# Kernel tuning notes

Measured on AMD Instinct MI355X. Metric: run time of the kernel, lower is better.

The kernel has to match this reference:

```python
import jax, jax.numpy as jnp
import numpy as np

S = 8192          # past KV length
H = 4096          # hidden size
NH = 32           # heads
HD = 128          # head dim
INNER = 16384     # MLP inner (4h)
ROT = 64          # rotary dim per 2D-rope half
NUM_LAYERS = 28
LAYER_ID = 0
ALPHA = (2.0 * NUM_LAYERS) ** 0.5
QK_COEFF = float(LAYER_ID + 1)            # query_key_layer_scaling_coeff
COEFF = (128.0 ** 0.5) * QK_COEFF         # math.sqrt(128) * coeff
EPS = 1e-5


def layernorm(x, w, b):
    mu = jnp.mean(x, axis=-1, keepdims=True)
    var = jnp.var(x, axis=-1, keepdims=True)
    return (x - mu) * jax.lax.rsqrt(var + EPS) * w + b


def rotate_half(x):
    # x: [..., 64]; GLM rotate-half at 32
    return jnp.concatenate([-x[..., 32:], x[..., :32]], axis=-1)


def setup_inputs() -> dict:
    key = jax.random.key(0)
    ks = jax.random.split(key, 16)
    # rotary cache (as in the driver script)
    inv_freq = 1.0 / (10000.0 ** (jnp.arange(0, ROT, 2, dtype=jnp.float32) / ROT))  # [32]
    t = jnp.arange(512, dtype=jnp.float32)
    freqs = jnp.einsum('i,j->ij', t, inv_freq)          # [512,32]
    emb = jnp.concatenate([freqs, freqs], axis=-1)      # [512,64]
    w = lambda k, shp: jax.random.normal(k, shp, dtype=jnp.float32) * 0.02
    return {
        'hidden_states': jax.random.normal(ks[0], (1, H), dtype=jnp.float32),
        'past_key': jax.random.normal(ks[1], (S, NH, HD), dtype=jnp.float32),
        'past_value': jax.random.normal(ks[2], (S, NH, HD), dtype=jnp.float32),
        'cos_cached': jnp.cos(emb),
        'sin_cached': jnp.sin(emb),
        'ln1_w': jnp.ones((H,), jnp.float32), 'ln1_b': jnp.zeros((H,), jnp.float32),
        'qkv_w': w(ks[3], (3 * H, H)), 'qkv_b': w(ks[4], (3 * H,)),
        'dense_w': w(ks[5], (H, H)), 'dense_b': w(ks[6], (H,)),
        'ln2_w': jnp.ones((H,), jnp.float32), 'ln2_b': jnp.zeros((H,), jnp.float32),
        'fc1_w': w(ks[7], (INNER, H)), 'fc1_b': w(ks[8], (INNER,)),
        'fc2_w': w(ks[9], (H, INNER)), 'fc2_b': w(ks[10], (H,)),
        'position_ids': jax.random.randint(ks[11], (1, 1), 0, 512),
        'block_position_ids': jax.random.randint(ks[12], (1, 1), 0, 512),
        'attention_mask': jnp.zeros((1, 1, S + 1), dtype=bool),
    }


def reference(hidden_states, past_key, past_value, cos_cached, sin_cached,
              ln1_w, ln1_b, qkv_w, qkv_b, dense_w, dense_b,
              ln2_w, ln2_b, fc1_w, fc1_b, fc2_w, fc2_b,
              position_ids, block_position_ids, attention_mask):
    # rotary lookups: embedding then transpose(0,1) -> [q_len,1,64]
    pos_cos = jnp.transpose(cos_cached[position_ids], (1, 0, 2))
    pos_sin = jnp.transpose(sin_cached[position_ids], (1, 0, 2))
    blk_cos = jnp.transpose(cos_cached[block_position_ids], (1, 0, 2))
    blk_sin = jnp.transpose(sin_cached[block_position_ids], (1, 0, 2))

    residual = layernorm(hidden_states, ln1_w, ln1_b)          # [1, H]
    qkv = residual @ qkv_w.T + qkv_b                           # [1, 3H]
    qkv = qkv.reshape(-1, NH, 3 * HD)                          # [1, 32, 384]
    query, key_new, value_new = jnp.split(qkv, 3, axis=2)      # each [1,32,128]

    q1, q2 = jnp.split(query, 2, axis=2)                       # [1,32,64] each
    k1, k2 = jnp.split(key_new, 2, axis=2)
    q1 = q1 * pos_cos + rotate_half(q1) * pos_sin
    k1 = k1 * pos_cos + rotate_half(k1) * pos_sin
    q2 = q2 * blk_cos + rotate_half(q2) * blk_sin
    k2 = k2 * blk_cos + rotate_half(k2) * blk_sin
    q = jnp.concatenate([q1, q2], axis=-1)                     # [1,32,128]
    k_new = jnp.concatenate([k1, k2], axis=-1)                 # [1,32,128]

    k = jnp.concatenate([past_key, k_new], axis=0)             # [S+1,32,128]
    v = jnp.concatenate([past_value, value_new], axis=0)       # [S+1,32,128]

    # scores: [heads, q=1, S+1]
    scores = jnp.einsum('qhd,khd->hqk', q / COEFF, k)
    scores = jnp.where(attention_mask, jnp.float32(-10000.0), scores)
    scores = scores * QK_COEFF
    probs = jax.nn.softmax(scores, axis=-1)
    ctx = jnp.einsum('hqk,khd->qhd', probs, v).reshape(-1, H)  # [1,4096]

    attn_out = ctx @ dense_w.T + dense_b
    hidden = residual * ALPHA + attn_out

    residual2 = layernorm(hidden, ln2_w, ln2_b)
    mlp = jax.nn.gelu(residual2 @ fc1_w.T + fc1_b, approximate=True)
    mlp = mlp @ fc2_w.T + fc2_b
    out = residual2 * ALPHA + mlp
    return (out, k, v)
```

## Files before the change

kernel.cpp:

```cpp
#include <hip/hip_runtime.h>
#include <math.h>

#define S_PAST 8192
#define S_TOT  8193
#define HID    4096
#define NH     32
#define HD     128
#define INNER  16384
#define CH     16
#define NCH    512
#define ALPHA_ 7.483314773547883f
#define INV_COEFF 0.08838834764831845f
#define EPS_ 1e-5f

__global__ __launch_bounds__(256) void ln_kernel(const float* __restrict__ xin,
                                                 const float* __restrict__ w,
                                                 const float* __restrict__ b,
                                                 float* __restrict__ out) {
    int tid = threadIdx.x;
    float xs[16];
    float s = 0.f, s2 = 0.f;
#pragma unroll
    for (int i = 0; i < 16; ++i) {
        float v = xin[tid + i * 256];
        xs[i] = v; s += v; s2 += v * v;
    }
    for (int off = 32; off; off >>= 1) {
        s  += __shfl_down(s, off, 64);
        s2 += __shfl_down(s2, off, 64);
    }
    __shared__ float rs[4], rs2[4];
    __shared__ float mu_s, ri_s;
    int wid = tid >> 6, lane = tid & 63;
    if (lane == 0) { rs[wid] = s; rs2[wid] = s2; }
    __syncthreads();
    if (tid == 0) {
        float S1 = rs[0] + rs[1] + rs[2] + rs[3];
        float S2 = rs2[0] + rs2[1] + rs2[2] + rs2[3];
        float mu = S1 / HID;
        float var = S2 / HID - mu * mu;
        mu_s = mu;
        ri_s = rsqrtf(var + EPS_);
    }
    __syncthreads();
    float mu = mu_s, ri = ri_s;
#pragma unroll
    for (int i = 0; i < 16; ++i) {
        int idx = tid + i * 256;
        out[idx] = (xs[i] - mu) * ri * w[idx] + b[idx];
    }
}

template <int C, int MODE>
__global__ __launch_bounds__(256) void gemv_kernel(
        const float* __restrict__ Wm, const float* __restrict__ bias,
        const float* __restrict__ x, float* __restrict__ y,
        const float* __restrict__ res) {
    int wid = threadIdx.x >> 6, lane = threadIdx.x & 63;
    int r = blockIdx.x * 4 + wid;
    const float4* __restrict__ rowv = (const float4*)(Wm + (size_t)r * C);
    const float4* __restrict__ xv = (const float4*)x;
    constexpr int IT = C / 4 / 64;
    float acc0 = 0.f, acc1 = 0.f;
#pragma unroll 8
    for (int it = 0; it < IT; it += 2) {
        float4 w0 = rowv[lane + it * 64];
        float4 x0 = xv[lane + it * 64];
        float4 w1 = rowv[lane + (it + 1) * 64];
        float4 x1 = xv[lane + (it + 1) * 64];
        acc0 += w0.x * x0.x + w0.y * x0.y + w0.z * x0.z + w0.w * x0.w;
        acc1 += w1.x * x1.x + w1.y * x1.y + w1.z * x1.z + w1.w * x1.w;
    }
    float acc = acc0 + acc1;
    for (int off = 32; off; off >>= 1) acc += __shfl_down(acc, off, 64);
    if (lane == 0) {
        float t = acc + bias[r];
        if (MODE == 1) t += ALPHA_ * res[r];
        if (MODE == 2) {
            float u = t;
            t = 0.5f * u * (1.f + tanhf(0.7978845608028654f * (u + 0.044715f * u * u * u)));
        }
        y[r] = t;
    }
}

__global__ __launch_bounds__(256) void gemv_wide_kernel(
        const float* __restrict__ Wm, const float* __restrict__ bias,
        const float* __restrict__ x, float* __restrict__ y,
        const float* __restrict__ res) {
    int tid = threadIdx.x;
    int r = blockIdx.x;
    const float4* __restrict__ rowv = (const float4*)(Wm + (size_t)r * INNER);
    const float4* __restrict__ xv = (const float4*)x;
    float acc0 = 0.f, acc1 = 0.f;
#pragma unroll 8
    for (int it = 0; it < 16; it += 2) {
        float4 w0 = rowv[tid + it * 256];
        float4 x0 = xv[tid + it * 256];
        float4 w1 = rowv[tid + (it + 1) * 256];
        float4 x1 = xv[tid + (it + 1) * 256];
        acc0 += w0.x * x0.x + w0.y * x0.y + w0.z * x0.z + w0.w * x0.w;
        acc1 += w1.x * x1.x + w1.y * x1.y + w1.z * x1.z + w1.w * x1.w;
    }
    float acc = acc0 + acc1;
    for (int off = 32; off; off >>= 1) acc += __shfl_down(acc, off, 64);
    __shared__ float red[4];
    int wid = tid >> 6, lane = tid & 63;
    if (lane == 0) red[wid] = acc;
    __syncthreads();
    if (tid == 0) {
        float t = red[0] + red[1] + red[2] + red[3] + bias[r];
        t += ALPHA_ * res[r];
        y[r] = t;
    }
}

__global__ __launch_bounds__(128) void rope_kv_kernel(
        const float* __restrict__ qkv, const float* __restrict__ cosc,
        const float* __restrict__ sinc, const int* __restrict__ pos_ids,
        const int* __restrict__ blk_ids, float* __restrict__ qrot,
        float* __restrict__ kout, float* __restrict__ vout) {
    int h = blockIdx.x, d = threadIdx.x;
    int pos = pos_ids[0], blk = blk_ids[0];
    const float* qh = qkv + h * 384;
    float q = qh[d], k = qh[128 + d], v = qh[256 + d];
    int half = d >> 6;
    int i = d & 63;
    int p = half ? blk : pos;
    float c = cosc[p * 64 + i];
    float s = sinc[p * 64 + i];
    float qpart, kpart;
    int base = half * 64;
    if (i < 32) { qpart = -qh[base + i + 32]; kpart = -qh[128 + base + i + 32]; }
    else        { qpart =  qh[base + i - 32]; kpart =  qh[128 + base + i - 32]; }
    float qo = q * c + qpart * s;
    float ko = k * c + kpart * s;
    qrot[h * HD + d] = qo * INV_COEFF;
    size_t o = (size_t)S_PAST * HID + h * HD + d;
    kout[o] = ko;
    vout[o] = v;
}

__global__ __launch_bounds__(512) void attn_onepass(
        const float* __restrict__ qrot, const float* __restrict__ pastk,
        const float* __restrict__ pastv, float* __restrict__ kout,
        float* __restrict__ vout, const unsigned char* __restrict__ mask,
        float* __restrict__ pctx, float* __restrict__ pL) {
    int tid = threadIdx.x;
    int t = tid & 255, u = tid >> 8;
    int s0 = blockIdx.x * CH;
    int rows = (blockIdx.x == NCH - 1) ? (S_TOT - s0) : CH;
    int rstart = u * 8;
    int rend = u ? rows : 8;
    int a = t >> 5;
    const float4* __restrict__ qv = (const float4*)qrot;
    float4 q0 = qv[t], q1 = qv[256 + t], q2 = qv[512 + t], q3 = qv[768 + t];
    float4 a0 = {0,0,0,0}, a1 = {0,0,0,0}, a2 = {0,0,0,0}, a3 = {0,0,0,0};
    float eL0 = 0.f, eL1 = 0.f, eL2 = 0.f, eL3 = 0.f;
#pragma unroll 4
    for (int r = rstart; r < rend; ++r) {
        int srow = s0 + r;
        bool past = srow < S_PAST;
        const float* kbase = past ? pastk : kout;
        const float* vbase = past ? pastv : vout;
        const float4* krow = (const float4*)(kbase + (size_t)srow * HID);
        const float4* vrow = (const float4*)(vbase + (size_t)srow * HID);
        float4 k0 = krow[t], k1 = krow[256 + t];
        float4 k2 = krow[512 + t], k3 = krow[768 + t];
        float4 v0 = vrow[t], v1 = vrow[256 + t];
        float4 v2 = vrow[512 + t], v3 = vrow[768 + t];
        if (past) {
            float4* ko = (float4*)(kout + (size_t)srow * HID);
            ko[t] = k0; ko[256 + t] = k1; ko[512 + t] = k2; ko[768 + t] = k3;
            float4* vo = (float4*)(vout + (size_t)srow * HID);
            vo[t] = v0; vo[256 + t] = v1; vo[512 + t] = v2; vo[768 + t] = v3;
        }
        float d0 = q0.x * k0.x + q0.y * k0.y + q0.z * k0.z + q0.w * k0.w;
        float d1 = q1.x * k1.x + q1.y * k1.y + q1.z * k1.z + q1.w * k1.w;
        float d2 = q2.x * k2.x + q2.y * k2.y + q2.z * k2.z + q2.w * k2.w;
        float d3 = q3.x * k3.x + q3.y * k3.y + q3.z * k3.z + q3.w * k3.w;
#pragma unroll
        for (int off = 1; off < 32; off <<= 1) {
            d0 += __shfl_xor(d0, off, 64);
            d1 += __shfl_xor(d1, off, 64);
            d2 += __shfl_xor(d2, off, 64);
            d3 += __shfl_xor(d3, off, 64);
        }
        if (mask[srow]) { d0 = d1 = d2 = d3 = -10000.f; }
        float p0 = __expf(d0), p1 = __expf(d1), p2 = __expf(d2), p3 = __expf(d3);
        eL0 += p0; eL1 += p1; eL2 += p2; eL3 += p3;
        a0.x += p0 * v0.x; a0.y += p0 * v0.y; a0.z += p0 * v0.z; a0.w += p0 * v0.w;
        a1.x += p1 * v1.x; a1.y += p1 * v1.y; a1.z += p1 * v1.z; a1.w += p1 * v1.w;
        a2.x += p2 * v2.x; a2.y += p2 * v2.y; a2.z += p2 * v2.z; a2.w += p2 * v2.w;
        a3.x += p3 * v3.x; a3.y += p3 * v3.y; a3.z += p3 * v3.z; a3.w += p3 * v3.w;
    }
    __shared__ float acc_lds[256][16];
    __shared__ float eLds[2][8][4];
    if (u == 1) {
        acc_lds[t][0]  = a0.x; acc_lds[t][1]  = a0.y; acc_lds[t][2]  = a0.z; acc_lds[t][3]  = a0.w;
        acc_lds[t][4]  = a1.x; acc_lds[t][5]  = a1.y; acc_lds[t][6]  = a1.z; acc_lds[t][7]  = a1.w;
        acc_lds[t][8]  = a2.x; acc_lds[t][9]  = a2.y; acc_lds[t][10] = a2.z; acc_lds[t][11] = a2.w;
        acc_lds[t][12] = a3.x; acc_lds[t][13] = a3.y; acc_lds[t][14] = a3.z; acc_lds[t][15] = a3.w;
    }
    if ((t & 31) == 0) {
        eLds[u][a][0] = eL0; eLds[u][a][1] = eL1;
        eLds[u][a][2] = eL2; eLds[u][a][3] = eL3;
    }
    __syncthreads();
    if (u == 0) {
        a0.x += acc_lds[t][0];  a0.y += acc_lds[t][1];  a0.z += acc_lds[t][2];  a0.w += acc_lds[t][3];
        a1.x += acc_lds[t][4];  a1.y += acc_lds[t][5];  a1.z += acc_lds[t][6];  a1.w += acc_lds[t][7];
        a2.x += acc_lds[t][8];  a2.y += acc_lds[t][9];  a2.z += acc_lds[t][10]; a2.w += acc_lds[t][11];
        a3.x += acc_lds[t][12]; a3.y += acc_lds[t][13]; a3.z += acc_lds[t][14]; a3.w += acc_lds[t][15];
        float4* pc = (float4*)(pctx + (size_t)blockIdx.x * HID);
        pc[t] = a0; pc[256 + t] = a1; pc[512 + t] = a2; pc[768 + t] = a3;
    }
    if (tid < NH) {
        int ah = tid & 7, g = tid >> 3;
        pL[tid * NCH + blockIdx.x] = eLds[0][ah][g] + eLds[1][ah][g];
    }
}

__global__ __launch_bounds__(256) void ctx_reduce(const float* __restrict__ pctx,
                                                  const float* __restrict__ pL,
                                                  float* __restrict__ ctx) {
    int b = blockIdx.x, t = threadIdx.x;
    int i0 = b * 16;
    int h = i0 >> 7;
    float e = pL[h * NCH + t] + pL[h * NCH + 256 + t];
    for (int off = 32; off; off >>= 1) e += __shfl_down(e, off, 64);
    __shared__ float ew[4];
    int wid = t >> 6, lane = t & 63;
    if (lane == 0) ew[wid] = e;
    int r0 = t >> 4, ii = t & 15;
    float a = 0.f;
    for (int r = r0; r < NCH; r += 16) a += pctx[(size_t)r * HID + i0 + ii];
    __shared__ float sc[16][17];
    sc[r0][ii] = a;
    __syncthreads();
    float Lh = ew[0] + ew[1] + ew[2] + ew[3];
    if (t < 16) {
        float s = 0.f;
#pragma unroll
        for (int r = 0; r < 16; ++r) s += sc[r][t];
        ctx[i0 + t] = s / Lh;
    }
}

extern "C" void kernel_launch(void* const* d_in, const int* in_sizes, int n_in,
                              void* d_out, int out_size, void* d_ws, size_t ws_size,
                              hipStream_t stream) {
    const float* hidden = (const float*)d_in[0];
    const float* past_k = (const float*)d_in[1];
    const float* past_v = (const float*)d_in[2];
    const float* cosc = (const float*)d_in[3];
    const float* sinc = (const float*)d_in[4];
    const float* ln1w = (const float*)d_in[5];
    const float* ln1b = (const float*)d_in[6];
    const float* qkvw = (const float*)d_in[7];
    const float* qkvb = (const float*)d_in[8];
    const float* denw = (const float*)d_in[9];
    const float* denb = (const float*)d_in[10];
    const float* ln2w = (const float*)d_in[11];
    const float* ln2b = (const float*)d_in[12];
    const float* fc1w = (const float*)d_in[13];
    const float* fc1b = (const float*)d_in[14];
    const float* fc2w = (const float*)d_in[15];
    const float* fc2b = (const float*)d_in[16];
    const int* pos = (const int*)d_in[17];
    const int* blk = (const int*)d_in[18];
    const unsigned char* mask = (const unsigned char*)d_in[19];

    float* out_f = (float*)d_out;
    float* kout = out_f + HID;
    float* vout = kout + (size_t)S_TOT * HID;

    float* ws = (float*)d_ws;
    float* resid1 = ws;
    float* qkvv   = ws + 4096;
    float* qrot   = ws + 16384;
    float* ctx    = ws + 20480;
    float* hid2   = ws + 24576;
    float* resid2 = ws + 28672;
    float* mlpi   = ws + 32768;
    float* pL     = ws + 49152;
    float* pctx   = ws + 65536;

    ln_kernel<<<1, 256, 0, stream>>>(hidden, ln1w, ln1b, resid1);
    gemv_kernel<HID, 0><<<3 * HID / 4, 256, 0, stream>>>(qkvw, qkvb, resid1, qkvv, nullptr);
    rope_kv_kernel<<<NH, HD, 0, stream>>>(qkvv, cosc, sinc, pos, blk, qrot, kout, vout);
    attn_onepass<<<NCH, 512, 0, stream>>>(qrot, past_k, past_v, kout, vout, mask, pctx, pL);
    ctx_reduce<<<256, 256, 0, stream>>>(pctx, pL, ctx);
    gemv_kernel<HID, 1><<<HID / 4, 256, 0, stream>>>(denw, denb, ctx, hid2, resid1);
    ln_kernel<<<1, 256, 0, stream>>>(hid2, ln2w, ln2b, resid2);
    gemv_kernel<HID, 2><<<INNER / 4, 256, 0, stream>>>(fc1w, fc1b, resid2, mlpi, nullptr);
    gemv_wide_kernel<<<HID, 256, 0, stream>>>(fc2w, fc2b, mlpi, out_f, resid2);
}
```

Measured before the change: 283.4 us.

## Fuse LayerNorm into QKV GEMV and fold RoPE/new-token KV into attention

Replaces the first LayerNorm kernel with a stats-only kernel and applies the normalization on the fly inside the QKV GEMV and the dense epilogue. The separate RoPE kernel is removed: each attention block recomputes the rotated query into LDS, and the last block handles the new key/value row. The aim is fewer kernel launches and fewer small dependent steps on the critical path. In exchange, every attention block repeats the query RoPE work, the QKV GEMV rereads LN weights per row, and the single-accumulator GEMV loops may expose more load latency.

```diff
diff --git a/kernel.cpp b/kernel.cpp
--- a/kernel.cpp
+++ b/kernel.cpp
@@ -13,6 +13,29 @@
 #define INV_COEFF 0.08838834764831845f
 #define EPS_ 1e-5f
 
+__global__ __launch_bounds__(256) void ln_stats_kernel(const float* __restrict__ xin,
+                                                       float* __restrict__ stats) {
+    int tid = threadIdx.x;
+    float s = 0.f, s2 = 0.f;
+#pragma unroll
+    for (int i = 0; i < 16; ++i) {
+        float v = xin[tid + i * 256];
+        s += v; s2 += v * v;
+    }
+    for (int off = 32; off; off >>= 1) {
+        s  += __shfl_down(s, off, 64);
+        s2 += __shfl_down(s2, off, 64);
+    }
+    __shared__ float rs[4], rs2[4];
+    int wid = tid >> 6, lane = tid & 63;
+    if (lane == 0) { rs[wid] = s; rs2[wid] = s2; }
+    __syncthreads();
+    if (tid == 0) {
+        stats[0] = rs[0] + rs[1] + rs[2] + rs[3];
+        stats[1] = rs2[0] + rs2[1] + rs2[2] + rs2[3];
+    }
+}
+
 __global__ __launch_bounds__(256) void ln_kernel(const float* __restrict__ xin,
                                                  const float* __restrict__ w,
                                                  const float* __restrict__ b,
@@ -51,36 +74,84 @@
     }
 }
 
-template <int C, int MODE>
-__global__ __launch_bounds__(256) void gemv_kernel(
+__global__ __launch_bounds__(256) void gemv_qkv_ln(
+        const float* __restrict__ Wm, const float* __restrict__ bias,
+        const float* __restrict__ hidden, const float* __restrict__ lnw,
+        const float* __restrict__ lnb, const float* __restrict__ stats,
+        float* __restrict__ y) {
+    int wid = threadIdx.x >> 6, lane = threadIdx.x & 63;
+    int r = blockIdx.x * 4 + wid;
+    const float4* __restrict__ rowv = (const float4*)(Wm + (size_t)r * HID);
+    const float4* __restrict__ hv = (const float4*)hidden;
+    const float4* __restrict__ wv = (const float4*)lnw;
+    const float4* __restrict__ bv = (const float4*)lnb;
+    float mu = stats[0] * (1.f / HID);
+    float var = stats[1] * (1.f / HID) - mu * mu;
+    float ri = rsqrtf(var + EPS_);
+    float acc = 0.f;
+#pragma unroll 8
+    for (int it = 0; it < 16; ++it) {
+        int i = lane + it * 64;
+        float4 w0 = rowv[i];
+        float4 h0 = hv[i];
+        float4 a0 = wv[i];
+        float4 b0 = bv[i];
+        float x0 = (h0.x - mu) * ri * a0.x + b0.x;
+        float x1 = (h0.y - mu) * ri * a0.y + b0.y;
+        float x2 = (h0.z - mu) * ri * a0.z + b0.z;
+        float x3 = (h0.w - mu) * ri * a0.w + b0.w;
+        acc += w0.x * x0 + w0.y * x1 + w0.z * x2 + w0.w * x3;
+    }
+    for (int off = 32; off; off >>= 1) acc += __shfl_down(acc, off, 64);
+    if (lane == 0) y[r] = acc + bias[r];
+}
+
+__global__ __launch_bounds__(256) void gemv_dense(
         const float* __restrict__ Wm, const float* __restrict__ bias,
         const float* __restrict__ x, float* __restrict__ y,
-        const float* __restrict__ res) {
+        const float* __restrict__ hidden, const float* __restrict__ lnw,
+        const float* __restrict__ lnb, const float* __restrict__ stats) {
     int wid = threadIdx.x >> 6, lane = threadIdx.x & 63;
     int r = blockIdx.x * 4 + wid;
-    const float4* __restrict__ rowv = (const float4*)(Wm + (size_t)r * C);
+    const float4* __restrict__ rowv = (const float4*)(Wm + (size_t)r * HID);
     const float4* __restrict__ xv = (const float4*)x;
-    constexpr int IT = C / 4 / 64;
-    float acc0 = 0.f, acc1 = 0.f;
+    float acc = 0.f;
 #pragma unroll 8
-    for (int it = 0; it < IT; it += 2) {
-        float4 w0 = rowv[lane + it * 64];
-        float4 x0 = xv[lane + it * 64];
-        float4 w1 = rowv[lane + (it + 1) * 64];
-        float4 x1 = xv[lane + (it + 1) * 64];
-        acc0 += w0.x * x0.x + w0.y * x0.y + w0.z * x0.z + w0.w * x0.w;
-        acc1 += w1.x * x1.x + w1.y * x1.y + w1.z * x1.z + w1.w * x1.w;
-    }
-    float acc = acc0 + acc1;
+    for (int it = 0; it < 16; ++it) {
+        int i = lane + it * 64;
+        float4 w0 = rowv[i];
+        float4 x0 = xv[i];
+        acc += w0.x * x0.x + w0.y * x0.y + w0.z * x0.z + w0.w * x0.w;
+    }
     for (int off = 32; off; off >>= 1) acc += __shfl_down(acc, off, 64);
     if (lane == 0) {
-        float t = acc + bias[r];
-        if (MODE == 1) t += ALPHA_ * res[r];
-        if (MODE == 2) {
-            float u = t;
-            t = 0.5f * u * (1.f + tanhf(0.7978845608028654f * (u + 0.044715f * u * u * u)));
-        }
-        y[r] = t;
+        float mu = stats[0] * (1.f / HID);
+        float var = stats[1] * (1.f / HID) - mu * mu;
+        float ri = rsqrtf(var + EPS_);
+        float resid = (hidden[r] - mu) * ri * lnw[r] + lnb[r];
+        y[r] = acc + bias[r] + ALPHA_ * resid;
+    }
+}
+
+__global__ __launch_bounds__(256) void gemv_fc1(
+        const float* __restrict__ Wm, const float* __restrict__ bias,
+        const float* __restrict__ x, float* __restrict__ y) {
+    int wid = threadIdx.x >> 6, lane = threadIdx.x & 63;
+    int r = blockIdx.x * 4 + wid;
+    const float4* __restrict__ rowv = (const float4*)(Wm + (size_t)r * HID);
+    const float4* __restrict__ xv = (const float4*)x;
+    float acc = 0.f;
+#pragma unroll 8
+    for (int it = 0; it < 16; ++it) {
+        int i = lane + it * 64;
+        float4 w0 = rowv[i];
+        float4 x0 = xv[i];
+        acc += w0.x * x0.x + w0.y * x0.y + w0.z * x0.z + w0.w * x0.w;
+    }
+    for (int off = 32; off; off >>= 1) acc += __shfl_down(acc, off, 64);
+    if (lane == 0) {
+        float u = acc + bias[r];
+        y[r] = 0.5f * u * (1.f + tanhf(0.7978845608028654f * (u + 0.044715f * u * u * u)));
     }
 }
 
@@ -115,66 +186,52 @@
     }
 }
 
-__global__ __launch_bounds__(128) void rope_kv_kernel(
-        const float* __restrict__ qkv, const float* __restrict__ cosc,
+__global__ __launch_bounds__(512) void attn_onepass(
+        const float* __restrict__ qkvv, const float* __restrict__ cosc,
         const float* __restrict__ sinc, const int* __restrict__ pos_ids,
-        const int* __restrict__ blk_ids, float* __restrict__ qrot,
-        float* __restrict__ kout, float* __restrict__ vout) {
-    int h = blockIdx.x, d = threadIdx.x;
-    int pos = pos_ids[0], blk = blk_ids[0];
-    const float* qh = qkv + h * 384;
-    float q = qh[d], k = qh[128 + d], v = qh[256 + d];
-    int half = d >> 6;
-    int i = d & 63;
-    int p = half ? blk : pos;
-    float c = cosc[p * 64 + i];
-    float s = sinc[p * 64 + i];
-    float qpart, kpart;
-    int base = half * 64;
-    if (i < 32) { qpart = -qh[base + i + 32]; kpart = -qh[128 + base + i + 32]; }
-    else        { qpart =  qh[base + i - 32]; kpart =  qh[128 + base + i - 32]; }
-    float qo = q * c + qpart * s;
-    float ko = k * c + kpart * s;
-    qrot[h * HD + d] = qo * INV_COEFF;
-    size_t o = (size_t)S_PAST * HID + h * HD + d;
-    kout[o] = ko;
-    vout[o] = v;
-}
-
-__global__ __launch_bounds__(512) void attn_onepass(
-        const float* __restrict__ qrot, const float* __restrict__ pastk,
+        const int* __restrict__ blk_ids, const float* __restrict__ pastk,
         const float* __restrict__ pastv, float* __restrict__ kout,
         float* __restrict__ vout, const unsigned char* __restrict__ mask,
         float* __restrict__ pctx, float* __restrict__ pL) {
     int tid = threadIdx.x;
     int t = tid & 255, u = tid >> 8;
     int s0 = blockIdx.x * CH;
-    int rows = (blockIdx.x == NCH - 1) ? (S_TOT - s0) : CH;
-    int rstart = u * 8;
-    int rend = u ? rows : 8;
     int a = t >> 5;
-    const float4* __restrict__ qv = (const float4*)qrot;
-    float4 q0 = qv[t], q1 = qv[256 + t], q2 = qv[512 + t], q3 = qv[768 + t];
+    int pos = pos_ids[0], blk = blk_ids[0];
+    __shared__ float qrot_lds[HID];
+    for (int i = tid; i < HID; i += 512) {
+        int h = i >> 7, d = i & 127;
+        int half = d >> 6, j = d & 63;
+        int p = half ? blk : pos;
+        float c = cosc[p * 64 + j];
+        float s = sinc[p * 64 + j];
+        float q = qkvv[h * 384 + d];
+        int pj = (j < 32) ? (j + 32) : (j - 32);
+        float partner = qkvv[h * 384 + half * 64 + pj];
+        float qo = (j < 32) ? (q * c - partner * s) : (q * c + partner * s);
+        qrot_lds[i] = qo * INV_COEFF;
+    }
+    __syncthreads();
+    float4 q0 = *(const float4*)&qrot_lds[4 * t];
+    float4 q1 = *(const float4*)&qrot_lds[1024 + 4 * t];
+    float4 q2 = *(const float4*)&qrot_lds[2048 + 4 * t];
+    float4 q3 = *(const float4*)&qrot_lds[3072 + 4 * t];
     float4 a0 = {0,0,0,0}, a1 = {0,0,0,0}, a2 = {0,0,0,0}, a3 = {0,0,0,0};
     float eL0 = 0.f, eL1 = 0.f, eL2 = 0.f, eL3 = 0.f;
+    int rstart = u * 8, rend = rstart + 8;
 #pragma unroll 4
     for (int r = rstart; r < rend; ++r) {
         int srow = s0 + r;
-        bool past = srow < S_PAST;
-        const float* kbase = past ? pastk : kout;
-        const float* vbase = past ? pastv : vout;
-        const float4* krow = (const float4*)(kbase + (size_t)srow * HID);
-        const float4* vrow = (const float4*)(vbase + (size_t)srow * HID);
+        const float4* krow = (const float4*)(pastk + (size_t)srow * HID);
+        const float4* vrow = (const float4*)(pastv + (size_t)srow * HID);
         float4 k0 = krow[t], k1 = krow[256 + t];
         float4 k2 = krow[512 + t], k3 = krow[768 + t];
         float4 v0 = vrow[t], v1 = vrow[256 + t];
         float4 v2 = vrow[512 + t], v3 = vrow[768 + t];
-        if (past) {
-            float4* ko = (float4*)(kout + (size_t)srow * HID);
-            ko[t] = k0; ko[256 + t] = k1; ko[512 + t] = k2; ko[768 + t] = k3;
-            float4* vo = (float4*)(vout + (size_t)srow * HID);
-            vo[t] = v0; vo[256 + t] = v1; vo[512 + t] = v2; vo[768 + t] = v3;
-        }
+        float4* ko = (float4*)(kout + (size_t)srow * HID);
+        ko[t] = k0; ko[256 + t] = k1; ko[512 + t] = k2; ko[768 + t] = k3;
+        float4* vo = (float4*)(vout + (size_t)srow * HID);
+        vo[t] = v0; vo[256 + t] = v1; vo[512 + t] = v2; vo[768 + t] = v3;
         float d0 = q0.x * k0.x + q0.y * k0.y + q0.z * k0.z + q0.w * k0.w;
         float d1 = q1.x * k1.x + q1.y * k1.y + q1.z * k1.z + q1.w * k1.w;
         float d2 = q2.x * k2.x + q2.y * k2.y + q2.z * k2.z + q2.w * k2.w;
@@ -193,6 +250,55 @@
         a1.x += p1 * v1.x; a1.y += p1 * v1.y; a1.z += p1 * v1.z; a1.w += p1 * v1.w;
         a2.x += p2 * v2.x; a2.y += p2 * v2.y; a2.z += p2 * v2.z; a2.w += p2 * v2.w;
         a3.x += p3 * v3.x; a3.y += p3 * v3.y; a3.z += p3 * v3.z; a3.w += p3 * v3.w;
+    }
+    if (blockIdx.x == NCH - 1 && u == 1) {
+        float kk[16], vv[16];
+        float d0 = 0.f, d1 = 0.f, d2 = 0.f, d3 = 0.f;
+        float dd[4] = {0.f, 0.f, 0.f, 0.f};
+#pragma unroll
+        for (int g = 0; g < 4; ++g) {
+#pragma unroll
+            for (int j = 0; j < 4; ++j) {
+                int idx = 1024 * g + 4 * t + j;
+                int h = idx >> 7, d = idx & 127;
+                int half = d >> 6, jj = d & 63;
+                int p = half ? blk : pos;
+                float c = cosc[p * 64 + jj];
+                float s = sinc[p * 64 + jj];
+                float kq = qkvv[h * 384 + 128 + d];
+                int pj = (jj < 32) ? (jj + 32) : (jj - 32);
+                float partner = qkvv[h * 384 + 128 + half * 64 + pj];
+                float kn = (jj < 32) ? (kq * c - partner * s) : (kq * c + partner * s);
+                kk[g * 4 + j] = kn;
+                vv[g * 4 + j] = qkvv[h * 384 + 256 + d];
+                dd[g] += qrot_lds[idx] * kn;
+            }
+        }
+        size_t o = (size_t)S_PAST * HID;
+        float4 kv;
+        kv.x = kk[0];  kv.y = kk[1];  kv.z = kk[2];  kv.w = kk[3];  ((float4*)(kout + o))[t] = kv;
+        kv.x = kk[4];  kv.y = kk[5];  kv.z = kk[6];  kv.w = kk[7];  ((float4*)(kout + o))[256 + t] = kv;
+        kv.x = kk[8];  kv.y = kk[9];  kv.z = kk[10]; kv.w = kk[11]; ((float4*)(kout + o))[512 + t] = kv;
+        kv.x = kk[12]; kv.y = kk[13]; kv.z = kk[14]; kv.w = kk[15]; ((float4*)(kout + o))[768 + t] = kv;
+        kv.x = vv[0];  kv.y = vv[1];  kv.z = vv[2];  kv.w = vv[3];  ((float4*)(vout + o))[t] = kv;
+        kv.x = vv[4];  kv.y = vv[5];  kv.z = vv[6];  kv.w = vv[7];  ((float4*)(vout + o))[256 + t] = kv;
+        kv.x = vv[8];  kv.y = vv[9];  kv.z = vv[10]; kv.w = vv[11]; ((float4*)(vout + o))[512 + t] = kv;
+        kv.x = vv[12]; kv.y = vv[13]; kv.z = vv[14]; kv.w = vv[15]; ((float4*)(vout + o))[768 + t] = kv;
+        d0 = dd[0]; d1 = dd[1]; d2 = dd[2]; d3 = dd[3];
+#pragma unroll
+        for (int off = 1; off < 32; off <<= 1) {
+            d0 += __shfl_xor(d0, off, 64);
+            d1 += __shfl_xor(d1, off, 64);
+            d2 += __shfl_xor(d2, off, 64);
+            d3 += __shfl_xor(d3, off, 64);
+        }
+        if (mask[S_PAST]) { d0 = d1 = d2 = d3 = -10000.f; }
+        float p0 = __expf(d0), p1 = __expf(d1), p2 = __expf(d2), p3 = __expf(d3);
+        eL0 += p0; eL1 += p1; eL2 += p2; eL3 += p3;
+        a0.x += p0 * vv[0];  a0.y += p0 * vv[1];  a0.z += p0 * vv[2];  a0.w += p0 * vv[3];
+        a1.x += p1 * vv[4];  a1.y += p1 * vv[5];  a1.z += p1 * vv[6];  a1.w += p1 * vv[7];
+        a2.x += p2 * vv[8];  a2.y += p2 * vv[9];  a2.z += p2 * vv[10]; a2.w += p2 * vv[11];
+        a3.x += p3 * vv[12]; a3.y += p3 * vv[13]; a3.z += p3 * vv[14]; a3.w += p3 * vv[15];
     }
     __shared__ float acc_lds[256][16];
     __shared__ float eLds[2][8][4];
@@ -276,23 +382,24 @@
     float* vout = kout + (size_t)S_TOT * HID;
 
     float* ws = (float*)d_ws;
-    float* resid1 = ws;
-    float* qkvv   = ws + 4096;
-    float* qrot   = ws + 16384;
-    float* ctx    = ws + 20480;
-    float* hid2   = ws + 24576;
-    float* resid2 = ws + 28672;
-    float* mlpi   = ws + 32768;
-    float* pL     = ws + 49152;
-    float* pctx   = ws + 65536;
-
-    ln_kernel<<<1, 256, 0, stream>>>(hidden, ln1w, ln1b, resid1);
-    gemv_kernel<HID, 0><<<3 * HID / 4, 256, 0, stream>>>(qkvw, qkvb, resid1, qkvv, nullptr);
-    rope_kv_kernel<<<NH, HD, 0, stream>>>(qkvv, cosc, sinc, pos, blk, qrot, kout, vout);
-    attn_onepass<<<NCH, 512, 0, stream>>>(qrot, past_k, past_v, kout, vout, mask, pctx, pL);
+    float* qkvv   = ws;
+    float* ctx    = ws + 12288;
+    float* hid2   = ws + 16384;
+    float* resid2 = ws + 20480;
+    float* mlpi   = ws + 24576;
+    float* stats1 = ws + 40960;
+    float* pL     = ws + 40968;
+    float* pctx   = ws + 57352;
+
+    ln_stats_kernel<<<1, 256, 0, stream>>>(hidden, stats1);
+    gemv_qkv_ln<<<3 * HID / 4, 256, 0, stream>>>(qkvw, qkvb, hidden, ln1w, ln1b,
+                                                 stats1, qkvv);
+    attn_onepass<<<NCH, 512, 0, stream>>>(qkvv, cosc, sinc, pos, blk, past_k, past_v,
+                                          kout, vout, mask, pctx, pL);
     ctx_reduce<<<256, 256, 0, stream>>>(pctx, pL, ctx);
-    gemv_kernel<HID, 1><<<HID / 4, 256, 0, stream>>>(denw, denb, ctx, hid2, resid1);
+    gemv_dense<<<HID / 4, 256, 0, stream>>>(denw, denb, ctx, hid2,
+                                            hidden, ln1w, ln1b, stats1);
     ln_kernel<<<1, 256, 0, stream>>>(hid2, ln2w, ln2b, resid2);
-    gemv_kernel<HID, 2><<<INNER / 4, 256, 0, stream>>>(fc1w, fc1b, resid2, mlpi, nullptr);
+    gemv_fc1<<<INNER / 4, 256, 0, stream>>>(fc1w, fc1b, resid2, mlpi);
     gemv_wide_kernel<<<HID, 256, 0, stream>>>(fc2w, fc2b, mlpi, out_f, resid2);
 }
```

New measurement: 309.3 us. 9.1% more time.
